# Kernel tuning notes

Measured on AMD Instinct MI355X. Metric: run time of the kernel, lower is better.

Reference implementation:

```python
import jax, jax.numpy as jnp
import numpy as np

N_GRAPHS = 1024
N_NODES = 65536
N_EDGES = 262144
D = 256          # node/edge/global feature dim
D_IN = 3 * D     # concat of edge_agg, node_agg, globals
D_HID = 512
D_OUT = 256


def setup_inputs() -> dict:
    key = jax.random.key(0)
    ks = jax.random.split(key, 9)
    nodes = jax.random.normal(ks[0], (N_NODES, D), dtype=jnp.float32)
    edges = jax.random.normal(ks[1], (N_EDGES, D), dtype=jnp.float32)
    globals_ = jax.random.normal(ks[2], (N_GRAPHS, D), dtype=jnp.float32)
    node_graph_ids = jnp.sort(jax.random.randint(ks[3], (N_NODES,), 0, N_GRAPHS, dtype=jnp.int32))
    edge_graph_ids = jnp.sort(jax.random.randint(ks[4], (N_EDGES,), 0, N_GRAPHS, dtype=jnp.int32))
    W1 = jax.random.normal(ks[5], (D_IN, D_HID), dtype=jnp.float32) * (1.0 / np.sqrt(D_IN))
    b1 = jnp.zeros((D_HID,), dtype=jnp.float32)
    W2 = jax.random.normal(ks[6], (D_HID, D_OUT), dtype=jnp.float32) * (1.0 / np.sqrt(D_HID))
    b2 = jnp.zeros((D_OUT,), dtype=jnp.float32)
    return {"nodes": nodes, "edges": edges, "globals_": globals_,
            "node_graph_ids": node_graph_ids, "edge_graph_ids": edge_graph_ids,
            "W1": W1, "b1": b1, "W2": W2, "b2": b2}


def reference(nodes, edges, globals_, node_graph_ids, edge_graph_ids, W1, b1, W2, b2):
    G = globals_.shape[0]
    # EdgesToGlobalsAggregator / NodesToGlobalsAggregator: unsorted segment sum per graph
    edge_agg = jax.ops.segment_sum(edges, edge_graph_ids, num_segments=G)  # [G, D]
    node_agg = jax.ops.segment_sum(nodes, node_graph_ids, num_segments=G)  # [G, D]
    collected = jnp.concatenate([edge_agg, node_agg, globals_], axis=-1)   # [G, 3D]
    # global_model: 2-layer MLP with ReLU
    h = jax.nn.relu(collected @ W1 + b1)
    updated_globals = h @ W2 + b2
    return updated_globals
```

## Files before the change

kernel.cpp:

```cpp
#include <hip/hip_runtime.h>

#define G      1024
#define NNODES 65536
#define NEDGES 262144
#define D      256
#define DIN    768
#define DHID   512
#define DOUT   256

constexpr int EDGE_CHUNK  = 128;
constexpr int NODE_CHUNK  = 64;
constexpr int EDGE_BLOCKS = NEDGES / EDGE_CHUNK;
constexpr int NODE_BLOCKS = NNODES / NODE_CHUNK;
constexpr int COPY_BLOCKS = (G * D / 4) / 256;

__device__ __forceinline__ void flush_acc(float* __restrict__ dst, int col_off,
                                          int cur, int lane, float4& acc) {
    float* p = dst + (size_t)cur * DIN + col_off + lane * 4;
    atomicAdd(p + 0, acc.x); atomicAdd(p + 1, acc.y);
    atomicAdd(p + 2, acc.z); atomicAdd(p + 3, acc.w);
    acc.x = acc.y = acc.z = acc.w = 0.f;
}

__device__ __forceinline__ void seg_sum_rows(const float4* __restrict__ src,
                                             const int* __restrict__ ids,
                                             float* __restrict__ dst, int col_off,
                                             int r0, int nrows) {
    const int lane = threadIdx.x & 63;
    const int wave = threadIdx.x >> 6;
    const int per_wave = nrows >> 2;
    int r = r0 + wave * per_wave;
    const int rend = r + per_wave;

    float4 acc = {0.f, 0.f, 0.f, 0.f};
    int cur = ids[r];
    for (; r < rend; r += 8) {
        const int4 ia = *(const int4*)&ids[r];
        const int4 ib = *(const int4*)&ids[r + 4];
        float4 v0 = src[(size_t)(r + 0) * (D / 4) + lane];
        float4 v1 = src[(size_t)(r + 1) * (D / 4) + lane];
        float4 v2 = src[(size_t)(r + 2) * (D / 4) + lane];
        float4 v3 = src[(size_t)(r + 3) * (D / 4) + lane];
        float4 v4 = src[(size_t)(r + 4) * (D / 4) + lane];
        float4 v5 = src[(size_t)(r + 5) * (D / 4) + lane];
        float4 v6 = src[(size_t)(r + 6) * (D / 4) + lane];
        float4 v7 = src[(size_t)(r + 7) * (D / 4) + lane];
        if (ia.x == cur && ib.w == cur) {
            acc.x += v0.x + v1.x + v2.x + v3.x + v4.x + v5.x + v6.x + v7.x;
            acc.y += v0.y + v1.y + v2.y + v3.y + v4.y + v5.y + v6.y + v7.y;
            acc.z += v0.z + v1.z + v2.z + v3.z + v4.z + v5.z + v6.z + v7.z;
            acc.w += v0.w + v1.w + v2.w + v3.w + v4.w + v5.w + v6.w + v7.w;
        } else {
            const int idv[8] = {ia.x, ia.y, ia.z, ia.w, ib.x, ib.y, ib.z, ib.w};
            const float4 vv[8] = {v0, v1, v2, v3, v4, v5, v6, v7};
#pragma unroll
            for (int j = 0; j < 8; ++j) {
                if (idv[j] != cur) { flush_acc(dst, col_off, cur, lane, acc); cur = idv[j]; }
                acc.x += vv[j].x; acc.y += vv[j].y; acc.z += vv[j].z; acc.w += vv[j].w;
            }
        }
    }
    flush_acc(dst, col_off, cur, lane, acc);
}

__global__ __launch_bounds__(256) void aggregate_kernel(
        const float* __restrict__ nodes,
        const float* __restrict__ edges,
        const float* __restrict__ globals_,
        const int* __restrict__ nids,
        const int* __restrict__ eids,
        float* __restrict__ collected) {
    const int b = blockIdx.x;
    if (b < EDGE_BLOCKS) {
        seg_sum_rows((const float4*)edges, eids, collected, 0,
                     b * EDGE_CHUNK, EDGE_CHUNK);
    } else if (b < EDGE_BLOCKS + NODE_BLOCKS) {
        seg_sum_rows((const float4*)nodes, nids, collected, D,
                     (b - EDGE_BLOCKS) * NODE_CHUNK, NODE_CHUNK);
    } else {
        const int t = (b - EDGE_BLOCKS - NODE_BLOCKS) * 256 + threadIdx.x;
        const int g = t >> 6;
        const int c = t & 63;
        ((float4*)collected)[(size_t)g * (DIN / 4) + (2 * D / 4) + c] =
            ((const float4*)globals_)[t];
    }
}

template <int TM, int TN, int TK>
__global__ __launch_bounds__(256) void gemm_bias_act(
        const float* __restrict__ A, const float* __restrict__ B,
        const float* __restrict__ bias, float* __restrict__ C,
        int M, int N, int K, int relu) {
    __shared__ float As[TM][TK + 1];
    __shared__ __align__(16) float Bs[TK][TN];

    const int tid = threadIdx.x;
    const int tx = tid & 15;
    const int ty = tid >> 4;
    const int m0 = blockIdx.y * TM;
    const int n0 = blockIdx.x * TN;

    float4 acc0 = {0.f, 0.f, 0.f, 0.f};
    float4 acc1 = {0.f, 0.f, 0.f, 0.f};

    for (int kt = 0; kt < K; kt += TK) {
        {
            const int r = tid >> 3;
            const int c = (tid & 7) * 4;
            const float4 a4 = *(const float4*)&A[(size_t)(m0 + r) * K + kt + c];
            As[r][c] = a4.x; As[r][c + 1] = a4.y; As[r][c + 2] = a4.z; As[r][c + 3] = a4.w;
        }
        {
            const int r = tid >> 3;
            const int c = (tid & 7) * 8;
            *(float4*)&Bs[r][c]     = *(const float4*)&B[(size_t)(kt + r) * N + n0 + c];
            *(float4*)&Bs[r][c + 4] = *(const float4*)&B[(size_t)(kt + r) * N + n0 + c + 4];
        }
        __syncthreads();
#pragma unroll
        for (int k = 0; k < TK; ++k) {
            const float a0 = As[ty * 2 + 0][k];
            const float a1 = As[ty * 2 + 1][k];
            const float4 bv = *(const float4*)&Bs[k][tx * 4];
            acc0.x += a0 * bv.x; acc0.y += a0 * bv.y;
            acc0.z += a0 * bv.z; acc0.w += a0 * bv.w;
            acc1.x += a1 * bv.x; acc1.y += a1 * bv.y;
            acc1.z += a1 * bv.z; acc1.w += a1 * bv.w;
        }
        __syncthreads();
    }

    const int col = n0 + tx * 4;
    const int row = m0 + ty * 2;
    const float4 bv = *(const float4*)&bias[col];
    float4 o0, o1;
    o0.x = acc0.x + bv.x; o0.y = acc0.y + bv.y; o0.z = acc0.z + bv.z; o0.w = acc0.w + bv.w;
    o1.x = acc1.x + bv.x; o1.y = acc1.y + bv.y; o1.z = acc1.z + bv.z; o1.w = acc1.w + bv.w;
    if (relu) {
        o0.x = fmaxf(o0.x, 0.f); o0.y = fmaxf(o0.y, 0.f);
        o0.z = fmaxf(o0.z, 0.f); o0.w = fmaxf(o0.w, 0.f);
        o1.x = fmaxf(o1.x, 0.f); o1.y = fmaxf(o1.y, 0.f);
        o1.z = fmaxf(o1.z, 0.f); o1.w = fmaxf(o1.w, 0.f);
    }
    *(float4*)&C[(size_t)row * N + col] = o0;
    *(float4*)&C[(size_t)(row + 1) * N + col] = o1;
}

extern "C" void kernel_launch(void* const* d_in, const int* in_sizes, int n_in,
                              void* d_out, int out_size, void* d_ws, size_t ws_size,
                              hipStream_t stream) {
    const float* nodes    = (const float*)d_in[0];
    const float* edges    = (const float*)d_in[1];
    const float* globals_ = (const float*)d_in[2];
    const int*   nids     = (const int*)d_in[3];
    const int*   eids     = (const int*)d_in[4];
    const float* W1       = (const float*)d_in[5];
    const float* b1       = (const float*)d_in[6];
    const float* W2       = (const float*)d_in[7];
    const float* b2       = (const float*)d_in[8];
    float* out = (float*)d_out;

    float* collected = (float*)d_ws;
    float* h         = collected + (size_t)G * DIN;

    hipMemsetAsync(collected, 0, (size_t)G * DIN * sizeof(float), stream);

    aggregate_kernel<<<EDGE_BLOCKS + NODE_BLOCKS + COPY_BLOCKS, 256, 0, stream>>>(
        nodes, edges, globals_, nids, eids, collected);

    gemm_bias_act<32, 64, 32><<<dim3(DHID / 64, G / 32), 256, 0, stream>>>(
        collected, W1, b1, h, G, DHID, DIN, 1);

    gemm_bias_act<32, 64, 32><<<dim3(DOUT / 64, G / 32), 256, 0, stream>>>(
        h, W2, b2, out, G, DOUT, DHID, 0);
}
```

Measured before the change: 473.5 us.

## Replace atomic segment-sum with per-graph blocks using binary-searched segment bounds

Each block now owns one graph and finds its edge and node ranges by binary search over the sorted ids. It reduces those rows across four waves through shared memory and writes the full concatenated row directly. This removes the memset, the global atomics and the separate globals-copy path. In exchange, the grid shrinks to one block per graph with fewer loads in flight per wave, and work is imbalanced when graph sizes vary.

```diff
diff --git a/kernel.cpp b/kernel.cpp
--- a/kernel.cpp
+++ b/kernel.cpp
@@ -8,82 +8,82 @@
 #define DHID   512
 #define DOUT   256
 
-constexpr int EDGE_CHUNK  = 128;
-constexpr int NODE_CHUNK  = 64;
-constexpr int EDGE_BLOCKS = NEDGES / EDGE_CHUNK;
-constexpr int NODE_BLOCKS = NNODES / NODE_CHUNK;
-constexpr int COPY_BLOCKS = (G * D / 4) / 256;
-
-__device__ __forceinline__ void flush_acc(float* __restrict__ dst, int col_off,
-                                          int cur, int lane, float4& acc) {
-    float* p = dst + (size_t)cur * DIN + col_off + lane * 4;
-    atomicAdd(p + 0, acc.x); atomicAdd(p + 1, acc.y);
-    atomicAdd(p + 2, acc.z); atomicAdd(p + 3, acc.w);
-    acc.x = acc.y = acc.z = acc.w = 0.f;
+__device__ __forceinline__ int lower_bound(const int* __restrict__ a, int n, int key) {
+    int lo = 0, hi = n;
+    while (lo < hi) {
+        const int mid = (lo + hi) >> 1;
+        if (a[mid] < key) lo = mid + 1; else hi = mid;
+    }
+    return lo;
 }
 
-__device__ __forceinline__ void seg_sum_rows(const float4* __restrict__ src,
-                                             const int* __restrict__ ids,
-                                             float* __restrict__ dst, int col_off,
-                                             int r0, int nrows) {
-    const int lane = threadIdx.x & 63;
-    const int wave = threadIdx.x >> 6;
-    const int per_wave = nrows >> 2;
-    int r = r0 + wave * per_wave;
-    const int rend = r + per_wave;
-
-    float4 acc = {0.f, 0.f, 0.f, 0.f};
-    int cur = ids[r];
-    for (; r < rend; r += 8) {
-        const int4 ia = *(const int4*)&ids[r];
-        const int4 ib = *(const int4*)&ids[r + 4];
-        float4 v0 = src[(size_t)(r + 0) * (D / 4) + lane];
-        float4 v1 = src[(size_t)(r + 1) * (D / 4) + lane];
-        float4 v2 = src[(size_t)(r + 2) * (D / 4) + lane];
-        float4 v3 = src[(size_t)(r + 3) * (D / 4) + lane];
-        float4 v4 = src[(size_t)(r + 4) * (D / 4) + lane];
-        float4 v5 = src[(size_t)(r + 5) * (D / 4) + lane];
-        float4 v6 = src[(size_t)(r + 6) * (D / 4) + lane];
-        float4 v7 = src[(size_t)(r + 7) * (D / 4) + lane];
-        if (ia.x == cur && ib.w == cur) {
-            acc.x += v0.x + v1.x + v2.x + v3.x + v4.x + v5.x + v6.x + v7.x;
-            acc.y += v0.y + v1.y + v2.y + v3.y + v4.y + v5.y + v6.y + v7.y;
-            acc.z += v0.z + v1.z + v2.z + v3.z + v4.z + v5.z + v6.z + v7.z;
-            acc.w += v0.w + v1.w + v2.w + v3.w + v4.w + v5.w + v6.w + v7.w;
-        } else {
-            const int idv[8] = {ia.x, ia.y, ia.z, ia.w, ib.x, ib.y, ib.z, ib.w};
-            const float4 vv[8] = {v0, v1, v2, v3, v4, v5, v6, v7};
-#pragma unroll
-            for (int j = 0; j < 8; ++j) {
-                if (idv[j] != cur) { flush_acc(dst, col_off, cur, lane, acc); cur = idv[j]; }
-                acc.x += vv[j].x; acc.y += vv[j].y; acc.z += vv[j].z; acc.w += vv[j].w;
-            }
-        }
-    }
-    flush_acc(dst, col_off, cur, lane, acc);
-}
-
-__global__ __launch_bounds__(256) void aggregate_kernel(
-        const float* __restrict__ nodes,
-        const float* __restrict__ edges,
-        const float* __restrict__ globals_,
+__global__ __launch_bounds__(256) void fused_agg(
+        const float4* __restrict__ nodes,
+        const float4* __restrict__ edges,
+        const float4* __restrict__ globals_,
         const int* __restrict__ nids,
         const int* __restrict__ eids,
         float* __restrict__ collected) {
-    const int b = blockIdx.x;
-    if (b < EDGE_BLOCKS) {
-        seg_sum_rows((const float4*)edges, eids, collected, 0,
-                     b * EDGE_CHUNK, EDGE_CHUNK);
-    } else if (b < EDGE_BLOCKS + NODE_BLOCKS) {
-        seg_sum_rows((const float4*)nodes, nids, collected, D,
-                     (b - EDGE_BLOCKS) * NODE_CHUNK, NODE_CHUNK);
-    } else {
-        const int t = (b - EDGE_BLOCKS - NODE_BLOCKS) * 256 + threadIdx.x;
-        const int g = t >> 6;
-        const int c = t & 63;
-        ((float4*)collected)[(size_t)g * (DIN / 4) + (2 * D / 4) + c] =
-            ((const float4*)globals_)[t];
+    const int g    = blockIdx.x;
+    const int lane = threadIdx.x & 63;
+    const int wave = threadIdx.x >> 6;
+
+    const int es = lower_bound(eids, NEDGES, g);
+    const int ee = lower_bound(eids, NEDGES, g + 1);
+    const int ns = lower_bound(nids, NNODES, g);
+    const int ne = lower_bound(nids, NNODES, g + 1);
+
+    float4 acc_e = {0.f, 0.f, 0.f, 0.f};
+    {
+        int r = es + wave;
+        for (; r + 12 < ee; r += 16) {
+            const float4 v0 = edges[(size_t)(r +  0) * (D / 4) + lane];
+            const float4 v1 = edges[(size_t)(r +  4) * (D / 4) + lane];
+            const float4 v2 = edges[(size_t)(r +  8) * (D / 4) + lane];
+            const float4 v3 = edges[(size_t)(r + 12) * (D / 4) + lane];
+            acc_e.x += (v0.x + v1.x) + (v2.x + v3.x);
+            acc_e.y += (v0.y + v1.y) + (v2.y + v3.y);
+            acc_e.z += (v0.z + v1.z) + (v2.z + v3.z);
+            acc_e.w += (v0.w + v1.w) + (v2.w + v3.w);
+        }
+        for (; r < ee; r += 4) {
+            const float4 v = edges[(size_t)r * (D / 4) + lane];
+            acc_e.x += v.x; acc_e.y += v.y; acc_e.z += v.z; acc_e.w += v.w;
+        }
     }
+
+    float4 acc_n = {0.f, 0.f, 0.f, 0.f};
+    {
+        int r = ns + wave;
+        for (; r + 12 < ne; r += 16) {
+            const float4 v0 = nodes[(size_t)(r +  0) * (D / 4) + lane];
+            const float4 v1 = nodes[(size_t)(r +  4) * (D / 4) + lane];
+            const float4 v2 = nodes[(size_t)(r +  8) * (D / 4) + lane];
+            const float4 v3 = nodes[(size_t)(r + 12) * (D / 4) + lane];
+            acc_n.x += (v0.x + v1.x) + (v2.x + v3.x);
+            acc_n.y += (v0.y + v1.y) + (v2.y + v3.y);
+            acc_n.z += (v0.z + v1.z) + (v2.z + v3.z);
+            acc_n.w += (v0.w + v1.w) + (v2.w + v3.w);
+        }
+        for (; r < ne; r += 4) {
+            const float4 v = nodes[(size_t)r * (D / 4) + lane];
+            acc_n.x += v.x; acc_n.y += v.y; acc_n.z += v.z; acc_n.w += v.w;
+        }
+    }
+
+    __shared__ __align__(16) float se[4][D];
+    __shared__ __align__(16) float sn[4][D];
+    *(float4*)&se[wave][lane * 4] = acc_e;
+    *(float4*)&sn[wave][lane * 4] = acc_n;
+    __syncthreads();
+
+    const int t = threadIdx.x;
+    const float ev = (se[0][t] + se[1][t]) + (se[2][t] + se[3][t]);
+    const float nv = (sn[0][t] + sn[1][t]) + (sn[2][t] + sn[3][t]);
+    float* row = collected + (size_t)g * DIN;
+    row[t]           = ev;
+    row[D + t]       = nv;
+    row[2 * D + t]   = ((const float*)globals_)[(size_t)g * D + t];
 }
 
 template <int TM, int TN, int TK>
@@ -163,10 +163,9 @@
     float* collected = (float*)d_ws;
     float* h         = collected + (size_t)G * DIN;
 
-    hipMemsetAsync(collected, 0, (size_t)G * DIN * sizeof(float), stream);
-
-    aggregate_kernel<<<EDGE_BLOCKS + NODE_BLOCKS + COPY_BLOCKS, 256, 0, stream>>>(
-        nodes, edges, globals_, nids, eids, collected);
+    fused_agg<<<G, 256, 0, stream>>>(
+        (const float4*)nodes, (const float4*)edges, (const float4*)globals_,
+        nids, eids, collected);
 
     gemm_bias_act<32, 64, 32><<<dim3(DHID / 64, G / 32), 256, 0, stream>>>(
         collected, W1, b1, h, G, DHID, DIN, 1);
```

New measurement: 477.7 us. Within noise of the previous version (+0.9%).
